# Kernel tuning notes

Hardware: AMD Instinct MI355X
Metric: run time of the kernel (lower is better)

## Reference

```python
import jax, jax.numpy as jnp
import numpy as np

B, L, D, R = 8, 2048, 2048, 256
K = R if R % 2 == 1 else (R - 1 if R > 1 else 1)  # torch kernel-size rule -> 255


def setup_inputs() -> dict:
    key = jax.random.key(0)
    ks = jax.random.split(key, 6)
    x = jax.random.normal(ks[0], (B, L, D), dtype=jnp.float32)
    ln_gamma = jnp.ones((D,), jnp.float32)
    ln_beta = jnp.zeros((D,), jnp.float32)
    P_shared = jax.random.normal(ks[1], (D, R), jnp.float32) / np.float32(np.sqrt(D))
    dlt_T = jax.random.normal(ks[2], (R, R), jnp.float32) / np.float32(np.sqrt(R))
    phi_w = jax.random.normal(ks[3], (R,), jnp.float32)  # nn.Linear(1, r, bias=False) weight
    phi_bias = jnp.zeros((L, R), jnp.float32)            # created as zeros_like(phi_det)
    toep_params = jnp.ones((K,), jnp.float32) / np.float32(K)
    Wq = jax.random.normal(ks[4], (R, D), jnp.float32) / np.float32(np.sqrt(R))  # delta_Q: r->d
    bq = jnp.zeros((D,), jnp.float32)
    g_logit = jnp.array([-1.0, 0.0], jnp.float32)
    return {"x": x, "ln_gamma": ln_gamma, "ln_beta": ln_beta, "P_shared": P_shared,
            "dlt_T": dlt_T, "phi_w": phi_w, "phi_bias": phi_bias,
            "toep_params": toep_params, "Wq": Wq, "bq": bq, "g_logit": g_logit,
            "step": 5000}


def _layernorm(x, g, b, eps=1e-5):
    m = jnp.mean(x, -1, keepdims=True)
    v = jnp.mean((x - m) ** 2, -1, keepdims=True)
    return (x - m) * jax.lax.rsqrt(v + eps) * g + b


def _phi_det(Ll, Rr, dtype):
    # assumed phi_logic(t, L, r): DCT-II style deterministic phase table, shape (L, r)
    t = jnp.arange(Ll, dtype=dtype)[:, None]
    k = jnp.arange(Rr, dtype=dtype)[None, :]
    return jnp.cos(jnp.pi * (t + 0.5) * k / Ll)


def reference(x, ln_gamma, ln_beta, P_shared, dlt_T, phi_w, phi_bias,
              toep_params, Wq, bq, g_logit, step):
    Bb, Ll, Dd = x.shape
    Rr = P_shared.shape[1]
    x_norm = _layernorm(x, ln_gamma, ln_beta)
    phi_det = _phi_det(Ll, Rr, x.dtype)                      # (L, r)
    feat = jnp.mean(x_norm, -1, keepdims=True)               # (B, L, 1)
    phi_data = jnp.mean(feat * phi_w[None, None, :], axis=0)  # (L, r)
    det_scale = min(step / 2000.0, 1.0)                      # static Python scalar
    phi = det_scale * phi_det + phi_bias + phi_data          # (L, r)
    scale = jnp.sum(phi, axis=1) / jnp.float32(Rr)           # (L,)
    u = jnp.einsum('bld,dr->blr', x_norm, P_shared)          # SharedProj.forward_P
    z = jnp.einsum('blr,sr->bls', u, dlt_T)                  # DLT: fixed spectral transform
    # Toeplitz conv1d across spectral channels, padding 'same' (cross-correlation, as torch)
    zf = z.reshape(Bb * Ll, 1, Rr)
    mixed = jax.lax.conv_general_dilated(zf, toep_params[None, None, :], (1,), 'SAME',
                                         dimension_numbers=('NCH', 'OIH', 'NCH'))
    z_mixed = mixed.reshape(Bb, Ll, Rr)
    y = jnp.einsum('blr,rd->bld', z_mixed, Wq) + bq          # delta_Q
    g = jax.nn.sigmoid(g_logit)
    g = jnp.repeat(g, Dd // g.shape[0])                      # repeat_interleave to d_model
    # scale has L elements, broadcast over the FEATURE dim (L == d_model by construction)
    return g[None, None, :] * y * scale[None, None, :]
```

## Files before the change

kernel.cpp:

```cpp
#include <hip/hip_runtime.h>
#include <cstdint>
#include <math.h>

#define B_ 8
#define L_ 2048
#define D_ 2048
#define R_ 256

typedef __bf16 bf16x8 __attribute__((ext_vector_type(8)));
typedef float f32x4 __attribute__((ext_vector_type(4)));

__device__ __forceinline__ unsigned short f2bf(float f) {
    uint32_t u = __builtin_bit_cast(uint32_t, f);
    u += 0x7FFFu + ((u >> 16) & 1u);
    return (unsigned short)(u >> 16);
}

#define GLDS16(gp, lp)                                                          \
    __builtin_amdgcn_global_load_lds(                                           \
        (const __attribute__((address_space(1))) void*)(gp),                    \
        (__attribute__((address_space(3))) void*)(lp), 16, 0, 0)

__global__ __launch_bounds__(256) void ln_kernel(
    const float* __restrict__ x, const float* __restrict__ gamma,
    const float* __restrict__ beta, unsigned short* __restrict__ xn,
    float* __restrict__ feat)
{
    const int row  = blockIdx.x;
    const int t    = threadIdx.x;
    const int w    = t >> 6, lane = t & 63;
    const float4* x4 = (const float4*)(x + (size_t)row * D_);
    const float4* g4 = (const float4*)gamma;
    const float4* b4 = (const float4*)beta;
    float4 a  = x4[t];
    float4 b  = x4[t + 256];
    float4 g0 = g4[t], g1 = g4[t + 256];
    float4 e0 = b4[t], e1 = b4[t + 256];

    float s   = a.x + a.y + a.z + a.w + b.x + b.y + b.z + b.w;
    float sq  = a.x*a.x + a.y*a.y + a.z*a.z + a.w*a.w
              + b.x*b.x + b.y*b.y + b.z*b.z + b.w*b.w;
    float sxg = a.x*g0.x + a.y*g0.y + a.z*g0.z + a.w*g0.w
              + b.x*g1.x + b.y*g1.y + b.z*g1.z + b.w*g1.w;
    float sg  = g0.x + g0.y + g0.z + g0.w + g1.x + g1.y + g1.z + g1.w;
    float sb  = e0.x + e0.y + e0.z + e0.w + e1.x + e1.y + e1.z + e1.w;

    __shared__ float red[20];
#pragma unroll
    for (int o = 32; o; o >>= 1) {
        s   += __shfl_down(s, o);
        sq  += __shfl_down(sq, o);
        sxg += __shfl_down(sxg, o);
        sg  += __shfl_down(sg, o);
        sb  += __shfl_down(sb, o);
    }
    if (lane == 0) {
        red[w] = s; red[4+w] = sq; red[8+w] = sxg; red[12+w] = sg; red[16+w] = sb;
    }
    __syncthreads();
    float S    = red[0] + red[1] + red[2] + red[3];
    float SQ   = red[4] + red[5] + red[6] + red[7];
    float SXG  = red[8] + red[9] + red[10] + red[11];
    float SG   = red[12] + red[13] + red[14] + red[15];
    float SB   = red[16] + red[17] + red[18] + red[19];
    float mean = S * (1.0f / D_);
    float var  = SQ * (1.0f / D_) - mean * mean;
    float rstd = rsqrtf(var + 1e-5f);
    if (t == 0)
        feat[row] = (rstd * (SXG - mean * SG) + SB) * (1.0f / D_);

    float n[8];
    n[0] = (a.x - mean) * rstd * g0.x + e0.x;
    n[1] = (a.y - mean) * rstd * g0.y + e0.y;
    n[2] = (a.z - mean) * rstd * g0.z + e0.z;
    n[3] = (a.w - mean) * rstd * g0.w + e0.w;
    n[4] = (b.x - mean) * rstd * g1.x + e1.x;
    n[5] = (b.y - mean) * rstd * g1.y + e1.y;
    n[6] = (b.z - mean) * rstd * g1.z + e1.z;
    n[7] = (b.w - mean) * rstd * g1.w + e1.w;

    ushort4 o0, o1;
    o0.x = f2bf(n[0]); o0.y = f2bf(n[1]); o0.z = f2bf(n[2]); o0.w = f2bf(n[3]);
    o1.x = f2bf(n[4]); o1.y = f2bf(n[5]); o1.z = f2bf(n[6]); o1.w = f2bf(n[7]);
    ((ushort4*)(xn + (size_t)row * D_))[t]       = o0;
    ((ushort4*)(xn + (size_t)row * D_))[t + 256] = o1;
}

__global__ __launch_bounds__(256) void prep_kernel(
    const float* __restrict__ P, unsigned short* __restrict__ PT,
    const float* __restrict__ dlt, const float* __restrict__ toep,
    const float* __restrict__ Wq, unsigned short* __restrict__ WT,
    const float* __restrict__ phi_bias, const float* __restrict__ phi_w,
    const float* __restrict__ feat, const float* __restrict__ bq,
    const float* __restrict__ g_logit, const int* __restrict__ step,
    float* __restrict__ gs, float* __restrict__ bgs)
{
    __shared__ __align__(16) char smem[65536];
    const int bid = blockIdx.x;
    const int t   = threadIdx.x;

    if (bid < 32) {
        unsigned short* sT = (unsigned short*)smem;
        const int k0 = bid * 64;
#pragma unroll 8
        for (int j = 0; j < 64; j++)
            sT[j * 256 + t] = f2bf(P[(size_t)(k0 + j) * R_ + t]);
        __syncthreads();
#pragma unroll
        for (int c = 0; c < 16; c++) {
            ushort4 v;
            v.x = sT[(c * 4 + 0) * 256 + t];
            v.y = sT[(c * 4 + 1) * 256 + t];
            v.z = sT[(c * 4 + 2) * 256 + t];
            v.w = sT[(c * 4 + 3) * 256 + t];
            *(ushort4*)(PT + (size_t)t * D_ + k0 + c * 4) = v;
        }
    } else if (bid < 544) {
        float* C = (float*)smem;
        const int d0 = (bid - 32) * 4;
        {
            const int r  = t;
            int s0 = r - 127; if (s0 < 0) s0 = 0;
            int s1 = r + 127; if (s1 > 255) s1 = 255;
            float c0 = 0.f, c1 = 0.f, c2 = 0.f, c3 = 0.f;
            for (int s = s0; s <= s1; s++) {
                float tv = toep[r - s + 127];
                const float* wr = Wq + (size_t)s * D_ + d0;
                c0 += tv * wr[0]; c1 += tv * wr[1];
                c2 += tv * wr[2]; c3 += tv * wr[3];
            }
            C[r * 4 + 0] = c0; C[r * 4 + 1] = c1;
            C[r * 4 + 2] = c2; C[r * 4 + 3] = c3;
        }
        __syncthreads();
        {
            const int q = t;
            float a0 = 0.f, a1 = 0.f, a2 = 0.f, a3 = 0.f;
            for (int r = 0; r < 256; r++) {
                float dv = dlt[(size_t)r * R_ + q];
                a0 += dv * C[r * 4 + 0]; a1 += dv * C[r * 4 + 1];
                a2 += dv * C[r * 4 + 2]; a3 += dv * C[r * 4 + 3];
            }
            WT[(size_t)(d0 + 0) * R_ + q] = f2bf(a0);
            WT[(size_t)(d0 + 1) * R_ + q] = f2bf(a1);
            WT[(size_t)(d0 + 2) * R_ + q] = f2bf(a2);
            WT[(size_t)(d0 + 3) * R_ + q] = f2bf(a3);
        }
    } else {
        float* red = (float*)smem;
        const int l = bid - 544;
        const int k = t;
        const int w = k >> 6, lane = k & 63;
        float arg = 3.14159265358979323846f * ((float)l + 0.5f) * (float)k * (1.0f / L_);
        float cv = cosf(arg);
        float pb = phi_bias[(size_t)l * R_ + k];
        float pw = phi_w[k];
#pragma unroll
        for (int o = 32; o; o >>= 1) {
            cv += __shfl_down(cv, o);
            pb += __shfl_down(pb, o);
            pw += __shfl_down(pw, o);
        }
        if (lane == 0) { red[w] = cv; red[4 + w] = pb; red[8 + w] = pw; }
        __syncthreads();
        if (k == 0) {
            float cs  = red[0] + red[1] + red[2] + red[3];
            float pbs = red[4] + red[5] + red[6] + red[7];
            float pws = red[8] + red[9] + red[10] + red[11];
            float fb = 0.f;
            for (int b = 0; b < B_; b++) fb += feat[(size_t)b * L_ + l];
            fb *= (1.0f / B_);
            float det = fminf((float)step[0] / 2000.0f, 1.0f);
            float sc  = (det * cs + pbs + fb * pws) * (1.0f / R_);
            float gl  = g_logit[l >> 10];
            float gg  = 1.0f / (1.0f + expf(-gl));
            gs[l]  = gg * sc;
            bgs[l] = bq[l] * gg * sc;
        }
    }
}

__global__ __launch_bounds__(256, 2) void gemm1_kernel(
    const unsigned short* __restrict__ A,
    const unsigned short* __restrict__ BT,
    unsigned short* __restrict__ U)
{
    __shared__ __align__(16) unsigned short sA[2][2][128 * 32];
    __shared__ __align__(16) unsigned short sB[2][2][128 * 32];
    const int tid  = threadIdx.x;
    const int n0   = blockIdx.x * 128;
    const int m0   = blockIdx.y * 128;
    const int w    = tid >> 6, lane = tid & 63;
    const int quad = lane >> 4, m16 = lane & 15;
    const int wm   = (w >> 1) * 64, wn = (w & 1) * 64;
    const int ra   = tid >> 2, sa = tid & 3;

    const unsigned short* apb = A  + (size_t)(m0 + ra) * 2048 + sa * 8;
    const unsigned short* bpb = BT + (size_t)(n0 + ra) * 2048 + sa * 8;

    f32x4 acc[4][4] = {};

#define G1_STAGE(buf, kc)                                                       \
    do {                                                                        \
        _Pragma("unroll")                                                       \
        for (int h = 0; h < 2; h++) {                                           \
            GLDS16(apb + (kc) + h * 32,              &sA[buf][h][tid * 8]);     \
            GLDS16(apb + (kc) + h * 32 + 64 * 2048,  &sA[buf][h][2048 + tid * 8]); \
            GLDS16(bpb + (kc) + h * 32,              &sB[buf][h][tid * 8]);     \
            GLDS16(bpb + (kc) + h * 32 + 64 * 2048,  &sB[buf][h][2048 + tid * 8]); \
        }                                                                       \
    } while (0)

    G1_STAGE(0, 0);
    __syncthreads();

    int cur = 0;
    for (int kc = 0; kc < 2048; kc += 64) {
        if (kc + 64 < 2048) G1_STAGE(cur ^ 1, kc + 64);
#pragma unroll
        for (int h = 0; h < 2; h++) {
            bf16x8 af[4], bf[4];
#pragma unroll
            for (int i = 0; i < 4; i++)
                af[i] = *(const bf16x8*)(&sA[cur][h][(wm + i * 16 + m16) * 32 + quad * 8]);
#pragma unroll
            for (int j = 0; j < 4; j++)
                bf[j] = *(const bf16x8*)(&sB[cur][h][(wn + j * 16 + m16) * 32 + quad * 8]);
#pragma unroll
            for (int i = 0; i < 4; i++)
#pragma unroll
                for (int j = 0; j < 4; j++)
                    acc[i][j] = __builtin_amdgcn_mfma_f32_16x16x32_bf16(
                        af[i], bf[j], acc[i][j], 0, 0, 0);
        }
        __syncthreads();
        cur ^= 1;
    }
#undef G1_STAGE

#pragma unroll
    for (int i = 0; i < 4; i++)
#pragma unroll
        for (int j = 0; j < 4; j++) {
            int col = n0 + wn + j * 16 + m16;
#pragma unroll
            for (int r = 0; r < 4; r++) {
                int row = m0 + wm + i * 16 + quad * 4 + r;
                U[(size_t)row * 256 + col] = f2bf(acc[i][j][r]);
            }
        }
}

__global__ __launch_bounds__(256, 3) void gemm2_kernel(
    const unsigned short* __restrict__ A,
    const unsigned short* __restrict__ BT,
    const float* __restrict__ gs, const float* __restrict__ bgs,
    float* __restrict__ out)
{
    __shared__ __align__(16) unsigned short sA[2][128 * 32];
    __shared__ __align__(16) unsigned short sB[2][128 * 32];
    const int tid  = threadIdx.x;
    const int n0   = blockIdx.x * 128;
    const int m0   = blockIdx.y * 128;
    const int w    = tid >> 6, lane = tid & 63;
    const int quad = lane >> 4, m16 = lane & 15;
    const int wm   = (w >> 1) * 64, wn = (w & 1) * 64;
    const int ra   = tid >> 2, sa = tid & 3;

    const unsigned short* apb0 = A  + (size_t)(m0 + ra) * 256 + sa * 8;
    const unsigned short* apb1 = apb0 + (size_t)64 * 256;
    const unsigned short* bpb0 = BT + (size_t)(n0 + ra) * 256 + sa * 8;
    const unsigned short* bpb1 = bpb0 + (size_t)64 * 256;

    float gv[4], bv[4];
#pragma unroll
    for (int j = 0; j < 4; j++) {
        int col = n0 + wn + j * 16 + m16;
        gv[j] = gs[col];
        bv[j] = bgs[col];
    }

    f32x4 acc[4][4] = {};

#define G2_STAGE(buf, kc)                                      \
    do {                                                       \
        GLDS16(apb0 + (kc), &sA[buf][tid * 8]);                \
        GLDS16(apb1 + (kc), &sA[buf][(256 + tid) * 8]);        \
        GLDS16(bpb0 + (kc), &sB[buf][tid * 8]);                \
        GLDS16(bpb1 + (kc), &sB[buf][(256 + tid) * 8]);        \
    } while (0)

    G2_STAGE(0, 0);
    __syncthreads();

    int cur = 0;
    for (int kc = 0; kc < 256; kc += 32) {
        if (kc + 32 < 256) G2_STAGE(cur ^ 1, kc + 32);
        bf16x8 af[4], bf[4];
#pragma unroll
        for (int i = 0; i < 4; i++)
            af[i] = *(const bf16x8*)(&sA[cur][(wm + i * 16 + m16) * 32 + quad * 8]);
#pragma unroll
        for (int j = 0; j < 4; j++)
            bf[j] = *(const bf16x8*)(&sB[cur][(wn + j * 16 + m16) * 32 + quad * 8]);
#pragma unroll
        for (int i = 0; i < 4; i++)
#pragma unroll
            for (int j = 0; j < 4; j++)
                acc[i][j] = __builtin_amdgcn_mfma_f32_16x16x32_bf16(
                    af[i], bf[j], acc[i][j], 0, 0, 0);
        __syncthreads();
        cur ^= 1;
    }
#undef G2_STAGE

#pragma unroll
    for (int i = 0; i < 4; i++)
#pragma unroll
        for (int r = 0; r < 4; r++) {
            int row = m0 + wm + i * 16 + quad * 4 + r;
            float* op = out + (size_t)row * 2048 + n0 + wn;
#pragma unroll
            for (int j = 0; j < 4; j++)
                op[j * 16 + m16] = acc[i][j][r] * gv[j] + bv[j];
        }
}

extern "C" void kernel_launch(void* const* d_in, const int* in_sizes, int n_in,
                              void* d_out, int out_size, void* d_ws, size_t ws_size,
                              hipStream_t stream)
{
    const float* x        = (const float*)d_in[0];
    const float* ln_gamma = (const float*)d_in[1];
    const float* ln_beta  = (const float*)d_in[2];
    const float* P        = (const float*)d_in[3];
    const float* dlt      = (const float*)d_in[4];
    const float* phi_w    = (const float*)d_in[5];
    const float* phi_bias = (const float*)d_in[6];
    const float* toep     = (const float*)d_in[7];
    const float* Wq       = (const float*)d_in[8];
    const float* bq       = (const float*)d_in[9];
    const float* g_logit  = (const float*)d_in[10];
    const int*   step     = (const int*)d_in[11];
    float* out = (float*)d_out;

    char* w = (char*)d_ws;
    unsigned short* xn  = (unsigned short*)(w);
    unsigned short* u   = (unsigned short*)(w + 67108864);
    unsigned short* PT  = (unsigned short*)(w + 75497472);
    unsigned short* WT  = (unsigned short*)(w + 76546048);
    float*          feat= (float*)(w + 77856768);
    float*          gs  = (float*)(w + 77922304);
    float*          bgs = (float*)(w + 77930496);

    ln_kernel<<<dim3(B_ * L_), dim3(256), 0, stream>>>(x, ln_gamma, ln_beta, xn, feat);
    prep_kernel<<<dim3(2592), dim3(256), 0, stream>>>(P, PT, dlt, toep, Wq, WT,
                                                      phi_bias, phi_w, feat, bq,
                                                      g_logit, step, gs, bgs);
    gemm1_kernel<<<dim3(2, 128), dim3(256), 0, stream>>>(xn, PT, u);
    gemm2_kernel<<<dim3(16, 128), dim3(256), 0, stream>>>(u, WT, gs, bgs, out);
}
```

Baseline: 406.6 us.

## Split weight-folding prep into coalesced Toeplitz and DLT stages

```diff
diff --git a/kernel.cpp b/kernel.cpp
--- a/kernel.cpp
+++ b/kernel.cpp
@@ -86,16 +86,16 @@
     ((ushort4*)(xn + (size_t)row * D_))[t + 256] = o1;
 }
 
-__global__ __launch_bounds__(256) void prep_kernel(
+__global__ __launch_bounds__(256) void prep1_kernel(
     const float* __restrict__ P, unsigned short* __restrict__ PT,
-    const float* __restrict__ dlt, const float* __restrict__ toep,
-    const float* __restrict__ Wq, unsigned short* __restrict__ WT,
+    const float* __restrict__ toep, const float* __restrict__ Wq,
+    float* __restrict__ C,
     const float* __restrict__ phi_bias, const float* __restrict__ phi_w,
     const float* __restrict__ feat, const float* __restrict__ bq,
     const float* __restrict__ g_logit, const int* __restrict__ step,
     float* __restrict__ gs, float* __restrict__ bgs)
 {
-    __shared__ __align__(16) char smem[65536];
+    __shared__ __align__(16) char smem[32768];
     const int bid = blockIdx.x;
     const int t   = threadIdx.x;
 
@@ -115,40 +115,30 @@
             v.w = sT[(c * 4 + 3) * 256 + t];
             *(ushort4*)(PT + (size_t)t * D_ + k0 + c * 4) = v;
         }
-    } else if (bid < 544) {
-        float* C = (float*)smem;
-        const int d0 = (bid - 32) * 4;
-        {
-            const int r  = t;
-            int s0 = r - 127; if (s0 < 0) s0 = 0;
-            int s1 = r + 127; if (s1 > 255) s1 = 255;
-            float c0 = 0.f, c1 = 0.f, c2 = 0.f, c3 = 0.f;
-            for (int s = s0; s <= s1; s++) {
-                float tv = toep[r - s + 127];
-                const float* wr = Wq + (size_t)s * D_ + d0;
-                c0 += tv * wr[0]; c1 += tv * wr[1];
-                c2 += tv * wr[2]; c3 += tv * wr[3];
+    } else if (bid < 288) {
+        float* toepLds = (float*)smem;
+        const int cid = bid - 32;
+        const int r0  = (cid >> 3) * 8;
+        const int d   = (cid & 7) * 256 + t;
+        if (t < 255) toepLds[t] = toep[t];
+        __syncthreads();
+        float acc[8] = {};
+#pragma unroll 4
+        for (int s = 0; s < 256; s++) {
+            float wv = Wq[(size_t)s * D_ + d];
+#pragma unroll
+            for (int ri = 0; ri < 8; ri++) {
+                int idx = r0 + ri - s + 127;
+                if ((unsigned)idx < 255u)
+                    acc[ri] += toepLds[idx] * wv;
             }
-            C[r * 4 + 0] = c0; C[r * 4 + 1] = c1;
-            C[r * 4 + 2] = c2; C[r * 4 + 3] = c3;
-        }
-        __syncthreads();
-        {
-            const int q = t;
-            float a0 = 0.f, a1 = 0.f, a2 = 0.f, a3 = 0.f;
-            for (int r = 0; r < 256; r++) {
-                float dv = dlt[(size_t)r * R_ + q];
-                a0 += dv * C[r * 4 + 0]; a1 += dv * C[r * 4 + 1];
-                a2 += dv * C[r * 4 + 2]; a3 += dv * C[r * 4 + 3];
-            }
-            WT[(size_t)(d0 + 0) * R_ + q] = f2bf(a0);
-            WT[(size_t)(d0 + 1) * R_ + q] = f2bf(a1);
-            WT[(size_t)(d0 + 2) * R_ + q] = f2bf(a2);
-            WT[(size_t)(d0 + 3) * R_ + q] = f2bf(a3);
-        }
+        }
+#pragma unroll
+        for (int ri = 0; ri < 8; ri++)
+            C[(size_t)(r0 + ri) * D_ + d] = acc[ri];
     } else {
         float* red = (float*)smem;
-        const int l = bid - 544;
+        const int l = bid - 288;
         const int k = t;
         const int w = k >> 6, lane = k & 63;
         float arg = 3.14159265358979323846f * ((float)l + 0.5f) * (float)k * (1.0f / L_);
@@ -180,6 +170,24 @@
     }
 }
 
+__global__ __launch_bounds__(256) void prep2_kernel(
+    const float* __restrict__ dlt, const float* __restrict__ C,
+    unsigned short* __restrict__ WT)
+{
+    const int d0 = blockIdx.x * 2;
+    const int q  = threadIdx.x;
+    float a0 = 0.f, a1 = 0.f;
+#pragma unroll 8
+    for (int r = 0; r < 256; r++) {
+        float dv = dlt[(size_t)r * R_ + q];
+        const float* cr = C + (size_t)r * D_ + d0;
+        a0 += dv * cr[0];
+        a1 += dv * cr[1];
+    }
+    WT[(size_t)(d0 + 0) * R_ + q] = f2bf(a0);
+    WT[(size_t)(d0 + 1) * R_ + q] = f2bf(a1);
+}
+
 __global__ __launch_bounds__(256, 2) void gemm1_kernel(
     const unsigned short* __restrict__ A,
     const unsigned short* __restrict__ BT,
@@ -349,14 +357,16 @@
     unsigned short* u   = (unsigned short*)(w + 67108864);
     unsigned short* PT  = (unsigned short*)(w + 75497472);
     unsigned short* WT  = (unsigned short*)(w + 76546048);
-    float*          feat= (float*)(w + 77856768);
-    float*          gs  = (float*)(w + 77922304);
-    float*          bgs = (float*)(w + 77930496);
+    float*          C   = (float*)(w + 77594624);
+    float*          feat= (float*)(w + 79691776);
+    float*          gs  = (float*)(w + 79757312);
+    float*          bgs = (float*)(w + 79765504);
 
     ln_kernel<<<dim3(B_ * L_), dim3(256), 0, stream>>>(x, ln_gamma, ln_beta, xn, feat);
-    prep_kernel<<<dim3(2592), dim3(256), 0, stream>>>(P, PT, dlt, toep, Wq, WT,
-                                                      phi_bias, phi_w, feat, bq,
-                                                      g_logit, step, gs, bgs);
+    prep1_kernel<<<dim3(2336), dim3(256), 0, stream>>>(P, PT, toep, Wq, C,
+                                                       phi_bias, phi_w, feat, bq,
+                                                       g_logit, step, gs, bgs);
+    prep2_kernel<<<dim3(1024), dim3(256), 0, stream>>>(dlt, C, WT);
     gemm1_kernel<<<dim3(2, 128), dim3(256), 0, stream>>>(xn, PT, u);
     gemm2_kernel<<<dim3(16, 128), dim3(256), 0, stream>>>(u, WT, gs, bgs, out);
 }
```

Result: slower. 431.9 us (+6.2%).
